# Kernel tuning notes

Hardware: AMD Instinct MI355X
Metric: run time of the kernel (lower is better)

## Reference

```python
import jax, jax.numpy as jnp
import numpy as np

DIM = 384
COMP = 64          # mmcv CARAFEPack compressed_channels default
KK = 9             # up_kernel^2 (up_kernel=3)
S = 2              # scale_factor


def conv2d(x, w, b, pad):
    y = jax.lax.conv_general_dilated(
        x, w, window_strides=(1, 1), padding=((pad, pad), (pad, pad)),
        dimension_numbers=('NCHW', 'OIHW', 'NCHW'))
    return y + b[None, :, None, None]


def pixel_shuffle(x, s):
    b, c, h, w = x.shape
    x = x.reshape(b, c // (s * s), s, s, h, w)
    x = x.transpose(0, 1, 4, 2, 5, 3)  # b, c', h, s, w, s
    return x.reshape(b, c // (s * s), h * s, w * s)


def carafe_pack(x, cw, cb, ew, eb):
    # x: [b, c, h, w] -> [b, c, 2h, 2w]
    b, c, h, w = x.shape
    comp = conv2d(x, cw, cb, 0)          # [b, 64, h, w]
    mask = conv2d(comp, ew, eb, 1)       # [b, 36, h, w]
    mask = pixel_shuffle(mask, S)        # [b, 9, 2h, 2w]
    mask = jax.nn.softmax(mask, axis=1)  # normalize the 9 reassembly weights
    # unfold 3x3 neighborhoods of x (zero pad 1)
    xp = jnp.pad(x, ((0, 0), (0, 0), (1, 1), (1, 1)))
    patches = jnp.stack(
        [xp[:, :, di:di + h, dj:dj + w] for di in range(3) for dj in range(3)],
        axis=2)                          # [b, c, 9, h, w]
    # each high-res pixel (i,j) reads the low-res window at (i//2, j//2)
    mr = mask.reshape(b, KK, h, S, w, S)
    out = jnp.einsum('bckhw,bkhpwq->bchpwq', patches, mr)
    return out.reshape(b, c, h * S, w * S)


def bilinear_resize(x, h, w):
    b, c = x.shape[:2]
    return jax.image.resize(x, (b, c, h, w), method='bilinear')


def stage(src, guidance, cw, cb, ew, eb):
    h, w = src.shape[2], src.shape[3]
    g = bilinear_resize(guidance, h, w)
    up = carafe_pack(jnp.concatenate([src, g], axis=1), cw, cb, ew, eb)
    return up[:, :DIM]


def setup_inputs() -> dict:
    key = jax.random.key(0)
    ks = jax.random.split(key, 20)
    cin = DIM + 3
    d = {}
    d['source'] = jax.random.normal(ks[0], (4, DIM, 14, 14), jnp.float32)
    d['guidance'] = jax.random.normal(ks[1], (4, 3, 224, 224), jnp.float32)
    i = 2
    for name in ('up1', 'up2', 'up3', 'up4'):
        d[name + '_cw'] = jax.random.normal(ks[i], (COMP, cin, 1, 1), jnp.float32) / np.sqrt(cin); i += 1
        d[name + '_cb'] = jnp.zeros((COMP,), jnp.float32)
        d[name + '_ew'] = jax.random.normal(ks[i], (KK * S * S, COMP, 3, 3), jnp.float32) / np.sqrt(COMP * 9); i += 1
        d[name + '_eb'] = jnp.zeros((KK * S * S,), jnp.float32)
    d['proj_w'] = jax.random.normal(ks[i], (DIM, cin, 1, 1), jnp.float32) / np.sqrt(cin)
    d['proj_b'] = jnp.zeros((DIM,), jnp.float32)
    return d


def reference(source, guidance,
              up1_cw, up1_cb, up1_ew, up1_eb,
              up2_cw, up2_cb, up2_ew, up2_eb,
              up3_cw, up3_cb, up3_ew, up3_eb,
              up4_cw, up4_cb, up4_ew, up4_eb,
              proj_w, proj_b):
    s2 = stage(source, guidance, up1_cw, up1_cb, up1_ew, up1_eb)
    s4 = stage(s2, guidance, up2_cw, up2_cb, up2_ew, up2_eb)
    s8 = stage(s4, guidance, up3_cw, up3_cb, up3_ew, up3_eb)
    s16 = stage(s8, guidance, up4_cw, up4_cb, up4_ew, up4_eb)
    return conv2d(jnp.concatenate([s16, guidance], axis=1), proj_w, proj_b, 0)
```

## Files before the change

kernel.cpp:

```cpp
#include <hip/hip_runtime.h>
#include <cstdint>

#define BATCH 4
#define DIMC 384
#define CINC 387
#define COMPC 64
#define GSZ 224

typedef __attribute__((ext_vector_type(8))) short bf16x8;
typedef __attribute__((ext_vector_type(4))) short s16x4;
typedef __attribute__((ext_vector_type(4))) float f32x4;

static __device__ __forceinline__ unsigned short f2bf(float x) {
  unsigned int u = __float_as_uint(x);
  unsigned int r = (u + 0x7fffu + ((u >> 16) & 1u)) >> 16;
  return (unsigned short)r;
}
static __device__ __forceinline__ float bf2f(unsigned short b) {
  return __uint_as_float(((unsigned int)b) << 16);
}
static __device__ __forceinline__ void cvt2(float x, unsigned short& h, unsigned short& l) {
  unsigned int u = __float_as_uint(x);
  unsigned int hb = (u + 0x7fffu + ((u >> 16) & 1u)) >> 16;
  h = (unsigned short)hb;
  float r = x - __uint_as_float(hb << 16);
  unsigned int u2 = __float_as_uint(r);
  l = (unsigned short)((u2 + 0x7fffu + ((u2 >> 16) & 1u)) >> 16);
}

__global__ void resize_all(const float* __restrict__ g, float* __restrict__ o0,
                           float* __restrict__ o1, float* __restrict__ o2,
                           float* __restrict__ o3) {
  int s = blockIdx.y;
  int h = 14 << s;
  float* out = (s == 0) ? o0 : (s == 1) ? o1 : (s == 2) ? o2 : o3;
  int inv_scale = GSZ / h;
  int w = h;
  int idx = blockIdx.x * blockDim.x + threadIdx.x;
  int total = BATCH * 3 * h * w;
  if (idx >= total) return;
  int j = idx % w; int t = idx / w;
  int i = t % h; t /= h;
  float ks = (float)inv_scale;
  float sy = (i + 0.5f) * ks - 0.5f;
  float sx = (j + 0.5f) * ks - 0.5f;
  int y0 = (int)ceilf(sy - ks); if (y0 < 0) y0 = 0;
  int y1 = (int)floorf(sy + ks); if (y1 > GSZ - 1) y1 = GSZ - 1;
  int x0 = (int)ceilf(sx - ks); if (x0 < 0) x0 = 0;
  int x1 = (int)floorf(sx + ks); if (x1 > GSZ - 1) x1 = GSZ - 1;
  const float* gp = g + (size_t)t * GSZ * GSZ;
  float wsx = 0.f;
  for (int x = x0; x <= x1; ++x) wsx += fmaxf(0.f, 1.f - fabsf(sx - (float)x) / ks);
  float acc = 0.f, wsy = 0.f;
  for (int y = y0; y <= y1; ++y) {
    float wy = fmaxf(0.f, 1.f - fabsf(sy - (float)y) / ks);
    wsy += wy;
    if (wy > 0.f) {
      const float* rp = gp + (size_t)y * GSZ;
      float row = 0.f;
      for (int x = x0; x <= x1; ++x) {
        float wx = fmaxf(0.f, 1.f - fabsf(sx - (float)x) / ks);
        row += wx * rp[x];
      }
      acc += wy * row;
    }
  }
  out[idx] = acc / (wsx * wsy);
}

__global__ void prep_cw(const float* __restrict__ c0, const float* __restrict__ c1,
                        const float* __restrict__ c2, const float* __restrict__ c3,
                        float* __restrict__ cwT) {
  int s = blockIdx.y;
  const float* cw = (s == 0) ? c0 : (s == 1) ? c1 : (s == 2) ? c2 : c3;
  int idx = blockIdx.x * 256 + threadIdx.x;
  if (idx >= CINC * COMPC) return;
  int ci = idx >> 6, co = idx & 63;
  cwT[s * (CINC * COMPC) + idx] = cw[co * CINC + ci];
}

#define EW2_PER_S (4 * COMPC * 9 * 12)
__global__ void prep_ew(const float* __restrict__ e0, const float* __restrict__ e1,
                        const float* __restrict__ e2, const float* __restrict__ e3,
                        float* __restrict__ ewT2) {
  int s = blockIdx.y;
  const float* ew = (s == 0) ? e0 : (s == 1) ? e1 : (s == 2) ? e2 : e3;
  int idx = blockIdx.x * 256 + threadIdx.x;
  if (idx >= EW2_PER_S) return;
  int k = idx % 12; int r = idx / 12;
  int tap = r % 9; r /= 9;
  int ci = r % COMPC; int pos = r / COMPC;
  float val = 0.f;
  if (k < 9) val = ew[(size_t)(k * 4 + pos) * (COMPC * 9) + ci * 9 + tap];
  ewT2[(size_t)s * EW2_PER_S + idx] = val;
}

#define KPAD 416
__global__ void prep_w(const float* __restrict__ pw, short* __restrict__ Whi,
                       short* __restrict__ Wlo) {
  int idx = blockIdx.x * 256 + threadIdx.x;
  if (idx >= DIMC * KPAD) return;
  int co = idx / KPAD, k = idx % KPAD;
  float v = (k < CINC) ? pw[co * CINC + k] : 0.f;
  unsigned short hb = f2bf(v);
  Whi[idx] = (short)hb;
  Wlo[idx] = (short)f2bf(v - bf2f(hb));
}

__global__ void comp_conv_kernel(const float* __restrict__ src, const float* __restrict__ g,
                                 const float* __restrict__ cwT, const float* __restrict__ cb,
                                 float* __restrict__ comp, int h, int w) {
  int hw = h * w;
  int p = blockIdx.x * 256 + threadIdx.x;
  if (p >= hw) return;
  int co0 = blockIdx.y * 32;
  int n = blockIdx.z;
  float acc[32];
  #pragma unroll
  for (int c = 0; c < 32; ++c) acc[c] = cb[co0 + c];
  const float* sp = src + (size_t)n * DIMC * hw + p;
  const float* wbase = cwT + co0;
  for (int ci = 0; ci < DIMC; ++ci) {
    float v = sp[(size_t)ci * hw];
    const float* wr = wbase + ci * COMPC;
    #pragma unroll
    for (int c = 0; c < 32; c += 4) {
      float4 wv = *(const float4*)(wr + c);
      acc[c] += wv.x * v; acc[c + 1] += wv.y * v;
      acc[c + 2] += wv.z * v; acc[c + 3] += wv.w * v;
    }
  }
  const float* gp = g + (size_t)n * 3 * hw + p;
  #pragma unroll
  for (int ci = 0; ci < 3; ++ci) {
    float v = gp[(size_t)ci * hw];
    const float* wr = wbase + (DIMC + ci) * COMPC;
    #pragma unroll
    for (int c = 0; c < 32; c += 4) {
      float4 wv = *(const float4*)(wr + c);
      acc[c] += wv.x * v; acc[c + 1] += wv.y * v;
      acc[c + 2] += wv.z * v; acc[c + 3] += wv.w * v;
    }
  }
  float* op = comp + (size_t)n * COMPC * hw + p;
  #pragma unroll
  for (int c = 0; c < 32; ++c) op[(size_t)(co0 + c) * hw] = acc[c];
}

__global__ void enc_mask_kernel(const float* __restrict__ comp, const float* __restrict__ ewT2,
                                const float* __restrict__ eb, float* __restrict__ mask,
                                int h, int w) {
  int hw = h * w;
  int sw2 = w >> 1;
  int nstrip = h * sw2;
  int strip = blockIdx.x * 256 + threadIdx.x;
  if (strip >= nstrip) return;
  int pos = blockIdx.y;
  int n = blockIdx.z;
  int i = strip / sw2;
  int j0 = (strip - i * sw2) * 2;
  float acc[2][9];
  #pragma unroll
  for (int k = 0; k < 9; ++k) {
    float bv = eb[k * 4 + pos];
    acc[0][k] = bv; acc[1][k] = bv;
  }
  const float* cpn = comp + (size_t)n * COMPC * hw;
  const float* wpos = ewT2 + (size_t)pos * COMPC * 9 * 12;
  for (int ci = 0; ci < COMPC; ++ci) {
    const float* cp = cpn + (size_t)ci * hw;
    float v[3][4];
    #pragma unroll
    for (int di = 0; di < 3; ++di) {
      int y = i + di - 1;
      bool yok = (y >= 0 && y < h);
      #pragma unroll
      for (int xx = 0; xx < 4; ++xx) {
        int x = j0 - 1 + xx;
        v[di][xx] = (yok && x >= 0 && x < w) ? cp[(size_t)y * w + x] : 0.f;
      }
    }
    const float* wb = wpos + (size_t)ci * 9 * 12;
    #pragma unroll
    for (int tap = 0; tap < 9; ++tap) {
      int di = tap / 3, dj = tap % 3;
      float4 wa = *(const float4*)(wb + tap * 12);
      float4 wc = *(const float4*)(wb + tap * 12 + 4);
      float w8 = wb[tap * 12 + 8];
      #pragma unroll
      for (int px = 0; px < 2; ++px) {
        float val = v[di][dj + px];
        acc[px][0] += wa.x * val; acc[px][1] += wa.y * val;
        acc[px][2] += wa.z * val; acc[px][3] += wa.w * val;
        acc[px][4] += wc.x * val; acc[px][5] += wc.y * val;
        acc[px][6] += wc.z * val; acc[px][7] += wc.w * val;
        acc[px][8] += w8 * val;
      }
    }
  }
  int pp = pos >> 1, q = pos & 1;
  int H = 2 * h, W = 2 * w;
  #pragma unroll
  for (int px = 0; px < 2; ++px) {
    int jj = j0 + px;
    float m = -1e30f;
    #pragma unroll
    for (int k = 0; k < 9; ++k) m = fmaxf(m, acc[px][k]);
    float e[9]; float s = 0.f;
    #pragma unroll
    for (int k = 0; k < 9; ++k) { e[k] = __expf(acc[px][k] - m); s += e[k]; }
    float inv = 1.f / s;
    float* mp = mask + (((size_t)n * H + (2 * i + pp)) * W + (2 * jj + q)) * 9;
    #pragma unroll
    for (int k = 0; k < 9; ++k) mp[k] = e[k] * inv;
  }
}

__global__ void carafe_kernel(const float* __restrict__ src, const float* __restrict__ mask,
                              float* __restrict__ out, int h, int w) {
  int p = blockIdx.x * blockDim.x + threadIdx.x;
  int hw = h * w;
  if (p >= hw) return;
  int c0 = blockIdx.y * 48, n = blockIdx.z;
  int i = p / w, j = p % w;
  int H = 2 * h, W = 2 * w;
  float m[4][9];
  #pragma unroll
  for (int pp = 0; pp < 2; ++pp)
    #pragma unroll
    for (int q = 0; q < 2; ++q) {
      const float* mp = mask + (((size_t)n * H + (2 * i + pp)) * W + (2 * j + q)) * 9;
      #pragma unroll
      for (int k = 0; k < 9; ++k) m[pp * 2 + q][k] = mp[k];
    }
  for (int cc = 0; cc < 48; ++cc) {
    int c = c0 + cc;
    const float* sp = src + ((size_t)(n * DIMC + c)) * hw;
    float v[9];
    #pragma unroll
    for (int k = 0; k < 9; ++k) {
      int y = i - 1 + k / 3, x = j - 1 + k % 3;
      v[k] = (y >= 0 && y < h && x >= 0 && x < w) ? sp[(size_t)y * w + x] : 0.f;
    }
    float* op = out + ((size_t)(n * DIMC + c)) * H * W;
    #pragma unroll
    for (int pp = 0; pp < 2; ++pp) {
      float a0 = 0.f, a1 = 0.f;
      #pragma unroll
      for (int k = 0; k < 9; ++k) {
        a0 += v[k] * m[pp * 2 + 0][k];
        a1 += v[k] * m[pp * 2 + 1][k];
      }
      float2 r; r.x = a0; r.y = a1;
      *(float2*)(op + (size_t)(2 * i + pp) * W + 2 * j) = r;
    }
  }
}

__global__ __launch_bounds__(512, 4) void final_conv_mfma4(
    const float* __restrict__ guid, const short* __restrict__ Whi,
    const short* __restrict__ Wlo, const float* __restrict__ pb,
    float* __restrict__ out) {
  __shared__ short XH[2][2048];
  __shared__ short XL[2][2048];
  const int HW = GSZ * GSZ;
  const int n = blockIdx.y;
  const int px0 = blockIdx.x * 64;
  const int tid = threadIdx.x;
  const int wv = tid >> 6;
  const int lane = tid & 63;
  const int lm = lane & 15, qq = lane >> 4;

  const int s_nt = lane >> 4, s_lm = lane & 15;
  const int s_qq = wv >> 1;
  const int s_jh = (wv & 1) * 4;
  const int waddr = ((s_nt * 4 + s_qq) * 16 + s_lm) * 8 + s_jh;

  const float* Xb = out + (size_t)n * DIMC * HW + px0 + lane;
  const float* Gb = guid + (size_t)n * 3 * HW + px0 + lane;

  f32x4 acc[3][4];
  #pragma unroll
  for (int mt = 0; mt < 3; ++mt)
    #pragma unroll
    for (int nt = 0; nt < 4; ++nt) acc[mt][nt] = (f32x4){0.f, 0.f, 0.f, 0.f};

  float nvA[4];
  bf16x8 ahC[3], alC[3];
  {
    unsigned short hs[4], ls[4];
    #pragma unroll
    for (int i = 0; i < 4; ++i) {
      float v = Xb[(size_t)(wv * 4 + i) * HW];
      cvt2(v, hs[i], ls[i]);
    }
    *(s16x4*)&XH[0][waddr] = (s16x4){(short)hs[0], (short)hs[1], (short)hs[2], (short)hs[3]};
    *(s16x4*)&XL[0][waddr] = (s16x4){(short)ls[0], (short)ls[1], (short)ls[2], (short)ls[3]};
    #pragma unroll
    for (int i = 0; i < 4; ++i) nvA[i] = Xb[(size_t)(32 + wv * 4 + i) * HW];
    #pragma unroll
    for (int mt = 0; mt < 3; ++mt) {
      int co = wv * 48 + mt * 16 + lm;
      size_t woff = (size_t)co * KPAD + qq * 8;
      ahC[mt] = *(const bf16x8*)(Whi + woff);
      alC[mt] = *(const bf16x8*)(Wlo + woff);
    }
  }
  __syncthreads();

  #pragma unroll
  for (int kt = 0; kt < 13; ++kt) {
    const int cur = kt & 1;
    bf16x8 ahN[3], alN[3];
    if (kt < 12) {
      #pragma unroll
      for (int mt = 0; mt < 3; ++mt) {
        int co = wv * 48 + mt * 16 + lm;
        size_t woff = (size_t)co * KPAD + (kt + 1) * 32 + qq * 8;
        ahN[mt] = *(const bf16x8*)(Whi + woff);
        alN[mt] = *(const bf16x8*)(Wlo + woff);
      }
    }
    float nvB[4] = {0.f, 0.f, 0.f, 0.f};
    if (kt <= 10) {
      int kb = (kt + 2) * 32 + wv * 4;
      if (kt < 10) {
        #pragma unroll
        for (int i = 0; i < 4; ++i) nvB[i] = Xb[(size_t)(kb + i) * HW];
      } else {
        #pragma unroll
        for (int i = 0; i < 4; ++i) {
          int k = kb + i;
          nvB[i] = (k < CINC) ? Gb[(size_t)(k - DIMC) * HW] : 0.f;
        }
      }
    }
    #pragma unroll
    for (int nt = 0; nt < 4; ++nt) {
      int a = ((nt * 4 + qq) * 16 + lm) * 8;
      bf16x8 bh = *(const bf16x8*)&XH[cur][a];
      bf16x8 bl = *(const bf16x8*)&XL[cur][a];
      #pragma unroll
      for (int mt = 0; mt < 3; ++mt) {
        acc[mt][nt] = __builtin_amdgcn_mfma_f32_16x16x32_bf16(ahC[mt], bh, acc[mt][nt], 0, 0, 0);
        acc[mt][nt] = __builtin_amdgcn_mfma_f32_16x16x32_bf16(ahC[mt], bl, acc[mt][nt], 0, 0, 0);
        acc[mt][nt] = __builtin_amdgcn_mfma_f32_16x16x32_bf16(alC[mt], bh, acc[mt][nt], 0, 0, 0);
      }
    }
    if (kt <= 11) {
      unsigned short hs[4], ls[4];
      #pragma unroll
      for (int i = 0; i < 4; ++i) cvt2(nvA[i], hs[i], ls[i]);
      *(s16x4*)&XH[cur ^ 1][waddr] = (s16x4){(short)hs[0], (short)hs[1], (short)hs[2], (short)hs[3]};
      *(s16x4*)&XL[cur ^ 1][waddr] = (s16x4){(short)ls[0], (short)ls[1], (short)ls[2], (short)ls[3]};
    }
    asm volatile("s_waitcnt lgkmcnt(0)" ::: "memory");
    __builtin_amdgcn_s_barrier();
    __builtin_amdgcn_sched_barrier(0);
    #pragma unroll
    for (int i = 0; i < 4; ++i) nvA[i] = nvB[i];
    if (kt < 12) {
      #pragma unroll
      for (int mt = 0; mt < 3; ++mt) { ahC[mt] = ahN[mt]; alC[mt] = alN[mt]; }
    }
  }

  #pragma unroll
  for (int mt = 0; mt < 3; ++mt) {
    #pragma unroll
    for (int nt = 0; nt < 4; ++nt) {
      #pragma unroll
      for (int r = 0; r < 4; ++r) {
        int co = wv * 48 + mt * 16 + qq * 4 + r;
        int px = px0 + nt * 16 + lm;
        out[((size_t)(n * DIMC + co)) * HW + px] = acc[mt][nt][r] + pb[co];
      }
    }
  }
}

extern "C" void kernel_launch(void* const* d_in, const int* in_sizes, int n_in,
                              void* d_out, int out_size, void* d_ws, size_t ws_size,
                              hipStream_t stream) {
  const float* source   = (const float*)d_in[0];
  const float* guidance = (const float*)d_in[1];
  const float* cw[4] = {(const float*)d_in[2],  (const float*)d_in[6],
                        (const float*)d_in[10], (const float*)d_in[14]};
  const float* cb[4] = {(const float*)d_in[3],  (const float*)d_in[7],
                        (const float*)d_in[11], (const float*)d_in[15]};
  const float* ew[4] = {(const float*)d_in[4],  (const float*)d_in[8],
                        (const float*)d_in[12], (const float*)d_in[16]};
  const float* eb[4] = {(const float*)d_in[5],  (const float*)d_in[9],
                        (const float*)d_in[13], (const float*)d_in[17]};
  const float* pw = (const float*)d_in[18];
  const float* pb = (const float*)d_in[19];
  float* out = (float*)d_out;

  float* ws = (float*)d_ws;
  float* g14  = ws;
  float* g28  = g14 + 2352;
  float* g56  = g28 + 9408;
  float* g112 = g56 + 37632;
  float* comp_buf = g112 + 150528;
  float* mask_buf = comp_buf + 3211264;
  float* s2  = mask_buf + 1806336;
  float* s4  = s2 + 1204224;
  float* s8  = s4 + 4816896;
  float* cwT = s8 + 19267584;
  float* ewT2 = cwT + 99072;
  short* Whi = (short*)(ewT2 + 110592);
  short* Wlo = Whi + DIMC * KPAD;

  prep_cw<<<dim3((CINC * COMPC + 255) / 256, 4), 256, 0, stream>>>(cw[0], cw[1], cw[2], cw[3], cwT);
  prep_ew<<<dim3((EW2_PER_S + 255) / 256, 4), 256, 0, stream>>>(ew[0], ew[1], ew[2], ew[3], ewT2);
  prep_w<<<(DIMC * KPAD + 255) / 256, 256, 0, stream>>>(pw, Whi, Wlo);
  resize_all<<<dim3((BATCH * 3 * 112 * 112 + 255) / 256, 4), 256, 0, stream>>>(
      guidance, g14, g28, g56, g112);

  const float* srcs[4] = {source, s2, s4, s8};
  float* outs[4] = {s2, s4, s8, out};
  float* gbufs[4] = {g14, g28, g56, g112};
  const int hs[4] = {14, 28, 56, 112};
  for (int s = 0; s < 4; ++s) {
    int h = hs[s], w = h, hw = h * w;
    int sw2 = w / 2;
    comp_conv_kernel<<<dim3((hw + 255) / 256, 2, BATCH), 256, 0, stream>>>(
        srcs[s], gbufs[s], cwT + s * (CINC * COMPC), cb[s], comp_buf, h, w);
    enc_mask_kernel<<<dim3((h * sw2 + 255) / 256, 4, BATCH), 256, 0, stream>>>(
        comp_buf, ewT2 + (size_t)s * EW2_PER_S, eb[s], mask_buf, h, w);
    carafe_kernel<<<dim3((hw + 255) / 256, DIMC / 48, BATCH), 256, 0, stream>>>(
        srcs[s], mask_buf, outs[s], h, w);
  }
  final_conv_mfma4<<<dim3((GSZ * GSZ) / 64, BATCH), 512, 0, stream>>>(guidance, Whi, Wlo, pb, out);
}
```

Measured before the change: 1.644 ms.

## Merge prep kernels, stage weights in LDS, template sizes, restructure final conv loop

Folds the four preprocessing kernels into one launch. It stages the compression and encoder weights in shared memory per block and templates the stage kernels on spatial size so indexing is compile-time. The final MFMA conv now loads A fragments per k-tile instead of prefetching them one step ahead, and uses a plain __syncthreads. This cuts launch count and repeated global weight reads, but the final conv loses its A-operand prefetch, which may expose load latency.

```diff
diff --git a/kernel.cpp b/kernel.cpp
--- a/kernel.cpp
+++ b/kernel.cpp
@@ -28,101 +28,107 @@
   l = (unsigned short)((u2 + 0x7fffu + ((u2 >> 16) & 1u)) >> 16);
 }
 
-__global__ void resize_all(const float* __restrict__ g, float* __restrict__ o0,
-                           float* __restrict__ o1, float* __restrict__ o2,
-                           float* __restrict__ o3) {
-  int s = blockIdx.y;
-  int h = 14 << s;
-  float* out = (s == 0) ? o0 : (s == 1) ? o1 : (s == 2) ? o2 : o3;
-  int inv_scale = GSZ / h;
-  int w = h;
-  int idx = blockIdx.x * blockDim.x + threadIdx.x;
-  int total = BATCH * 3 * h * w;
-  if (idx >= total) return;
-  int j = idx % w; int t = idx / w;
-  int i = t % h; t /= h;
-  float ks = (float)inv_scale;
-  float sy = (i + 0.5f) * ks - 0.5f;
-  float sx = (j + 0.5f) * ks - 0.5f;
-  int y0 = (int)ceilf(sy - ks); if (y0 < 0) y0 = 0;
-  int y1 = (int)floorf(sy + ks); if (y1 > GSZ - 1) y1 = GSZ - 1;
-  int x0 = (int)ceilf(sx - ks); if (x0 < 0) x0 = 0;
-  int x1 = (int)floorf(sx + ks); if (x1 > GSZ - 1) x1 = GSZ - 1;
-  const float* gp = g + (size_t)t * GSZ * GSZ;
-  float wsx = 0.f;
-  for (int x = x0; x <= x1; ++x) wsx += fmaxf(0.f, 1.f - fabsf(sx - (float)x) / ks);
-  float acc = 0.f, wsy = 0.f;
-  for (int y = y0; y <= y1; ++y) {
-    float wy = fmaxf(0.f, 1.f - fabsf(sy - (float)y) / ks);
-    wsy += wy;
-    if (wy > 0.f) {
-      const float* rp = gp + (size_t)y * GSZ;
-      float row = 0.f;
-      for (int x = x0; x <= x1; ++x) {
-        float wx = fmaxf(0.f, 1.f - fabsf(sx - (float)x) / ks);
-        row += wx * rp[x];
-      }
-      acc += wy * row;
-    }
-  }
-  out[idx] = acc / (wsx * wsy);
-}
-
-__global__ void prep_cw(const float* __restrict__ c0, const float* __restrict__ c1,
-                        const float* __restrict__ c2, const float* __restrict__ c3,
-                        float* __restrict__ cwT) {
-  int s = blockIdx.y;
-  const float* cw = (s == 0) ? c0 : (s == 1) ? c1 : (s == 2) ? c2 : c3;
+#define KPAD 416
+#define EW2_PER_S (4 * COMPC * 9 * 12)
+
+__global__ void prep_all(const float* __restrict__ c0, const float* __restrict__ c1,
+                         const float* __restrict__ c2, const float* __restrict__ c3,
+                         const float* __restrict__ e0, const float* __restrict__ e1,
+                         const float* __restrict__ e2, const float* __restrict__ e3,
+                         const float* __restrict__ pw,
+                         float* __restrict__ cwT, float* __restrict__ ewT2,
+                         short* __restrict__ Whi, short* __restrict__ Wlo,
+                         const float* __restrict__ g,
+                         float* __restrict__ r0, float* __restrict__ r1,
+                         float* __restrict__ r2, float* __restrict__ r3) {
+  int type = blockIdx.y;
   int idx = blockIdx.x * 256 + threadIdx.x;
-  if (idx >= CINC * COMPC) return;
-  int ci = idx >> 6, co = idx & 63;
-  cwT[s * (CINC * COMPC) + idx] = cw[co * CINC + ci];
-}
-
-#define EW2_PER_S (4 * COMPC * 9 * 12)
-__global__ void prep_ew(const float* __restrict__ e0, const float* __restrict__ e1,
-                        const float* __restrict__ e2, const float* __restrict__ e3,
-                        float* __restrict__ ewT2) {
-  int s = blockIdx.y;
-  const float* ew = (s == 0) ? e0 : (s == 1) ? e1 : (s == 2) ? e2 : e3;
-  int idx = blockIdx.x * 256 + threadIdx.x;
-  if (idx >= EW2_PER_S) return;
-  int k = idx % 12; int r = idx / 12;
-  int tap = r % 9; r /= 9;
-  int ci = r % COMPC; int pos = r / COMPC;
-  float val = 0.f;
-  if (k < 9) val = ew[(size_t)(k * 4 + pos) * (COMPC * 9) + ci * 9 + tap];
-  ewT2[(size_t)s * EW2_PER_S + idx] = val;
-}
-
-#define KPAD 416
-__global__ void prep_w(const float* __restrict__ pw, short* __restrict__ Whi,
-                       short* __restrict__ Wlo) {
-  int idx = blockIdx.x * 256 + threadIdx.x;
-  if (idx >= DIMC * KPAD) return;
-  int co = idx / KPAD, k = idx % KPAD;
-  float v = (k < CINC) ? pw[co * CINC + k] : 0.f;
-  unsigned short hb = f2bf(v);
-  Whi[idx] = (short)hb;
-  Wlo[idx] = (short)f2bf(v - bf2f(hb));
-}
-
+  if (type == 0) {
+    if (idx >= 4 * CINC * COMPC) return;
+    int s = idx / (CINC * COMPC), r = idx % (CINC * COMPC);
+    const float* cw = (s == 0) ? c0 : (s == 1) ? c1 : (s == 2) ? c2 : c3;
+    int ci = r >> 6, co = r & 63;
+    cwT[idx] = cw[co * CINC + ci];
+  } else if (type == 1) {
+    if (idx >= 4 * EW2_PER_S) return;
+    int s = idx / EW2_PER_S, r = idx % EW2_PER_S;
+    const float* ew = (s == 0) ? e0 : (s == 1) ? e1 : (s == 2) ? e2 : e3;
+    int k = r % 12; int rr = r / 12;
+    int tap = rr % 9; rr /= 9;
+    int ci = rr % COMPC; int pos = rr / COMPC;
+    float val = 0.f;
+    if (k < 9) val = ew[(size_t)(k * 4 + pos) * (COMPC * 9) + ci * 9 + tap];
+    ewT2[idx] = val;
+  } else if (type == 2) {
+    if (idx >= DIMC * KPAD) return;
+    int co = idx / KPAD, k = idx % KPAD;
+    float v = (k < CINC) ? pw[co * CINC + k] : 0.f;
+    unsigned short hb = f2bf(v);
+    Whi[idx] = (short)hb;
+    Wlo[idx] = (short)f2bf(v - bf2f(hb));
+  } else {
+    int s, base;
+    if (idx < 2352)        { s = 0; base = 0; }
+    else if (idx < 11760)  { s = 1; base = 2352; }
+    else if (idx < 49392)  { s = 2; base = 11760; }
+    else if (idx < 199920) { s = 3; base = 49392; }
+    else return;
+    int h = 14 << s, w = h;
+    float* out = (s == 0) ? r0 : (s == 1) ? r1 : (s == 2) ? r2 : r3;
+    int inv_scale = GSZ / h;
+    int local = idx - base;
+    int j = local % w; int t = local / w;
+    int i = t % h; t /= h;
+    float ks = (float)inv_scale;
+    float sy = (i + 0.5f) * ks - 0.5f;
+    float sx = (j + 0.5f) * ks - 0.5f;
+    int y0 = (int)ceilf(sy - ks); if (y0 < 0) y0 = 0;
+    int y1 = (int)floorf(sy + ks); if (y1 > GSZ - 1) y1 = GSZ - 1;
+    int x0 = (int)ceilf(sx - ks); if (x0 < 0) x0 = 0;
+    int x1 = (int)floorf(sx + ks); if (x1 > GSZ - 1) x1 = GSZ - 1;
+    const float* gp = g + (size_t)t * GSZ * GSZ;
+    float wsx = 0.f;
+    for (int x = x0; x <= x1; ++x) wsx += fmaxf(0.f, 1.f - fabsf(sx - (float)x) / ks);
+    float acc = 0.f, wsy = 0.f;
+    for (int y = y0; y <= y1; ++y) {
+      float wy = fmaxf(0.f, 1.f - fabsf(sy - (float)y) / ks);
+      wsy += wy;
+      if (wy > 0.f) {
+        const float* rp = gp + (size_t)y * GSZ;
+        float row = 0.f;
+        for (int x = x0; x <= x1; ++x) {
+          float wx = fmaxf(0.f, 1.f - fabsf(sx - (float)x) / ks);
+          row += wx * rp[x];
+        }
+        acc += wy * row;
+      }
+    }
+    out[local] = acc / (wsx * wsy);
+  }
+}
+
+template <int H>
 __global__ void comp_conv_kernel(const float* __restrict__ src, const float* __restrict__ g,
                                  const float* __restrict__ cwT, const float* __restrict__ cb,
-                                 float* __restrict__ comp, int h, int w) {
-  int hw = h * w;
+                                 float* __restrict__ comp) {
+  constexpr int hw = H * H;
+  __shared__ __align__(16) float WL[CINC * 32];
+  int co0 = blockIdx.y * 32;
+  for (int idx = threadIdx.x; idx < CINC * 32; idx += 256) {
+    int ci = idx >> 5, c = idx & 31;
+    WL[idx] = cwT[ci * COMPC + co0 + c];
+  }
+  __syncthreads();
   int p = blockIdx.x * 256 + threadIdx.x;
   if (p >= hw) return;
-  int co0 = blockIdx.y * 32;
   int n = blockIdx.z;
   float acc[32];
   #pragma unroll
   for (int c = 0; c < 32; ++c) acc[c] = cb[co0 + c];
   const float* sp = src + (size_t)n * DIMC * hw + p;
-  const float* wbase = cwT + co0;
   for (int ci = 0; ci < DIMC; ++ci) {
     float v = sp[(size_t)ci * hw];
-    const float* wr = wbase + ci * COMPC;
+    const float* wr = &WL[ci * 32];
     #pragma unroll
     for (int c = 0; c < 32; c += 4) {
       float4 wv = *(const float4*)(wr + c);
@@ -134,7 +140,7 @@
   #pragma unroll
   for (int ci = 0; ci < 3; ++ci) {
     float v = gp[(size_t)ci * hw];
-    const float* wr = wbase + (DIMC + ci) * COMPC;
+    const float* wr = &WL[(DIMC + ci) * 32];
     #pragma unroll
     for (int c = 0; c < 32; c += 4) {
       float4 wv = *(const float4*)(wr + c);
@@ -147,12 +153,18 @@
   for (int c = 0; c < 32; ++c) op[(size_t)(co0 + c) * hw] = acc[c];
 }
 
+template <int H>
 __global__ void enc_mask_kernel(const float* __restrict__ comp, const float* __restrict__ ewT2,
-                                const float* __restrict__ eb, float* __restrict__ mask,
-                                int h, int w) {
-  int hw = h * w;
-  int sw2 = w >> 1;
-  int nstrip = h * sw2;
+                                const float* __restrict__ eb, float* __restrict__ mask) {
+  constexpr int hw = H * H;
+  constexpr int sw2 = H / 2;
+  constexpr int nstrip = H * sw2;
+  __shared__ __align__(16) float WL[COMPC * 9 * 12];
+  {
+    const float* wpos = ewT2 + (size_t)blockIdx.y * (COMPC * 9 * 12);
+    for (int idx = threadIdx.x; idx < COMPC * 9 * 12; idx += 256) WL[idx] = wpos[idx];
+  }
+  __syncthreads();
   int strip = blockIdx.x * 256 + threadIdx.x;
   if (strip >= nstrip) return;
   int pos = blockIdx.y;
@@ -166,21 +178,20 @@
     acc[0][k] = bv; acc[1][k] = bv;
   }
   const float* cpn = comp + (size_t)n * COMPC * hw;
-  const float* wpos = ewT2 + (size_t)pos * COMPC * 9 * 12;
   for (int ci = 0; ci < COMPC; ++ci) {
     const float* cp = cpn + (size_t)ci * hw;
     float v[3][4];
     #pragma unroll
     for (int di = 0; di < 3; ++di) {
       int y = i + di - 1;
-      bool yok = (y >= 0 && y < h);
+      bool yok = (y >= 0 && y < H);
       #pragma unroll
       for (int xx = 0; xx < 4; ++xx) {
         int x = j0 - 1 + xx;
-        v[di][xx] = (yok && x >= 0 && x < w) ? cp[(size_t)y * w + x] : 0.f;
-      }
-    }
-    const float* wb = wpos + (size_t)ci * 9 * 12;
+        v[di][xx] = (yok && x >= 0 && x < H) ? cp[(size_t)y * H + x] : 0.f;
+      }
+    }
+    const float* wb = &WL[ci * 108];
     #pragma unroll
     for (int tap = 0; tap < 9; ++tap) {
       int di = tap / 3, dj = tap % 3;
@@ -199,7 +210,7 @@
     }
   }
   int pp = pos >> 1, q = pos & 1;
-  int H = 2 * h, W = 2 * w;
+  constexpr int W = 2 * H;
   #pragma unroll
   for (int px = 0; px < 2; ++px) {
     int jj = j0 + px;
@@ -210,26 +221,27 @@
     #pragma unroll
     for (int k = 0; k < 9; ++k) { e[k] = __expf(acc[px][k] - m); s += e[k]; }
     float inv = 1.f / s;
-    float* mp = mask + (((size_t)n * H + (2 * i + pp)) * W + (2 * jj + q)) * 9;
+    float* mp = mask + (((size_t)n * W + (2 * i + pp)) * W + (2 * jj + q)) * 9;
     #pragma unroll
     for (int k = 0; k < 9; ++k) mp[k] = e[k] * inv;
   }
 }
 
+template <int H>
 __global__ void carafe_kernel(const float* __restrict__ src, const float* __restrict__ mask,
-                              float* __restrict__ out, int h, int w) {
+                              float* __restrict__ out) {
+  constexpr int hw = H * H;
+  constexpr int W = 2 * H;
   int p = blockIdx.x * blockDim.x + threadIdx.x;
-  int hw = h * w;
   if (p >= hw) return;
   int c0 = blockIdx.y * 48, n = blockIdx.z;
-  int i = p / w, j = p % w;
-  int H = 2 * h, W = 2 * w;
+  int i = p / H, j = p % H;
   float m[4][9];
   #pragma unroll
   for (int pp = 0; pp < 2; ++pp)
     #pragma unroll
     for (int q = 0; q < 2; ++q) {
-      const float* mp = mask + (((size_t)n * H + (2 * i + pp)) * W + (2 * j + q)) * 9;
+      const float* mp = mask + (((size_t)n * W + (2 * i + pp)) * W + (2 * j + q)) * 9;
       #pragma unroll
       for (int k = 0; k < 9; ++k) m[pp * 2 + q][k] = mp[k];
     }
@@ -240,9 +252,9 @@
     #pragma unroll
     for (int k = 0; k < 9; ++k) {
       int y = i - 1 + k / 3, x = j - 1 + k % 3;
-      v[k] = (y >= 0 && y < h && x >= 0 && x < w) ? sp[(size_t)y * w + x] : 0.f;
-    }
-    float* op = out + ((size_t)(n * DIMC + c)) * H * W;
+      v[k] = (y >= 0 && y < H && x >= 0 && x < H) ? sp[(size_t)y * H + x] : 0.f;
+    }
+    float* op = out + ((size_t)(n * DIMC + c)) * W * W;
     #pragma unroll
     for (int pp = 0; pp < 2; ++pp) {
       float a0 = 0.f, a1 = 0.f;
@@ -257,7 +269,7 @@
   }
 }
 
-__global__ __launch_bounds__(512, 4) void final_conv_mfma4(
+__global__ __launch_bounds__(512, 4) void final_conv_mfma3(
     const float* __restrict__ guid, const short* __restrict__ Whi,
     const short* __restrict__ Wlo, const float* __restrict__ pb,
     float* __restrict__ out) {
@@ -286,7 +298,6 @@
     for (int nt = 0; nt < 4; ++nt) acc[mt][nt] = (f32x4){0.f, 0.f, 0.f, 0.f};
 
   float nvA[4];
-  bf16x8 ahC[3], alC[3];
   {
     unsigned short hs[4], ls[4];
     #pragma unroll
@@ -298,29 +309,32 @@
     *(s16x4*)&XL[0][waddr] = (s16x4){(short)ls[0], (short)ls[1], (short)ls[2], (short)ls[3]};
     #pragma unroll
     for (int i = 0; i < 4; ++i) nvA[i] = Xb[(size_t)(32 + wv * 4 + i) * HW];
+  }
+  __syncthreads();
+
+  for (int kt = 0; kt < 13; ++kt) {
+    const int cur = kt & 1;
+    bf16x8 bh[4], bl[4];
+    #pragma unroll
+    for (int nt = 0; nt < 4; ++nt) {
+      int a = ((nt * 4 + qq) * 16 + lm) * 8;
+      bh[nt] = *(const bf16x8*)&XH[cur][a];
+      bl[nt] = *(const bf16x8*)&XL[cur][a];
+    }
     #pragma unroll
     for (int mt = 0; mt < 3; ++mt) {
       int co = wv * 48 + mt * 16 + lm;
-      size_t woff = (size_t)co * KPAD + qq * 8;
-      ahC[mt] = *(const bf16x8*)(Whi + woff);
-      alC[mt] = *(const bf16x8*)(Wlo + woff);
-    }
-  }
-  __syncthreads();
-
-  #pragma unroll
-  for (int kt = 0; kt < 13; ++kt) {
-    const int cur = kt & 1;
-    bf16x8 ahN[3], alN[3];
-    if (kt < 12) {
-      #pragma unroll
-      for (int mt = 0; mt < 3; ++mt) {
-        int co = wv * 48 + mt * 16 + lm;
-        size_t woff = (size_t)co * KPAD + (kt + 1) * 32 + qq * 8;
-        ahN[mt] = *(const bf16x8*)(Whi + woff);
-        alN[mt] = *(const bf16x8*)(Wlo + woff);
-      }
-    }
+      size_t woff = (size_t)co * KPAD + kt * 32 + qq * 8;
+      bf16x8 ah = *(const bf16x8*)(Whi + woff);
+      bf16x8 al = *(const bf16x8*)(Wlo + woff);
+      #pragma unroll
+      for (int nt = 0; nt < 4; ++nt) {
+        acc[mt][nt] = __builtin_amdgcn_mfma_f32_16x16x32_bf16(ah, bh[nt], acc[mt][nt], 0, 0, 0);
+        acc[mt][nt] = __builtin_amdgcn_mfma_f32_16x16x32_bf16(ah, bl[nt], acc[mt][nt], 0, 0, 0);
+        acc[mt][nt] = __builtin_amdgcn_mfma_f32_16x16x32_bf16(al, bh[nt], acc[mt][nt], 0, 0, 0);
+      }
+    }
+    __builtin_amdgcn_sched_barrier(0);
     float nvB[4] = {0.f, 0.f, 0.f, 0.f};
     if (kt <= 10) {
       int kb = (kt + 2) * 32 + wv * 4;
@@ -335,18 +349,6 @@
         }
       }
     }
-    #pragma unroll
-    for (int nt = 0; nt < 4; ++nt) {
-      int a = ((nt * 4 + qq) * 16 + lm) * 8;
-      bf16x8 bh = *(const bf16x8*)&XH[cur][a];
-      bf16x8 bl = *(const bf16x8*)&XL[cur][a];
-      #pragma unroll
-      for (int mt = 0; mt < 3; ++mt) {
-        acc[mt][nt] = __builtin_amdgcn_mfma_f32_16x16x32_bf16(ahC[mt], bh, acc[mt][nt], 0, 0, 0);
-        acc[mt][nt] = __builtin_amdgcn_mfma_f32_16x16x32_bf16(ahC[mt], bl, acc[mt][nt], 0, 0, 0);
-        acc[mt][nt] = __builtin_amdgcn_mfma_f32_16x16x32_bf16(alC[mt], bh, acc[mt][nt], 0, 0, 0);
-      }
-    }
     if (kt <= 11) {
       unsigned short hs[4], ls[4];
       #pragma unroll
@@ -354,15 +356,9 @@
       *(s16x4*)&XH[cur ^ 1][waddr] = (s16x4){(short)hs[0], (short)hs[1], (short)hs[2], (short)hs[3]};
       *(s16x4*)&XL[cur ^ 1][waddr] = (s16x4){(short)ls[0], (short)ls[1], (short)ls[2], (short)ls[3]};
     }
-    asm volatile("s_waitcnt lgkmcnt(0)" ::: "memory");
-    __builtin_amdgcn_s_barrier();
-    __builtin_amdgcn_sched_barrier(0);
+    __syncthreads();
     #pragma unroll
     for (int i = 0; i < 4; ++i) nvA[i] = nvB[i];
-    if (kt < 12) {
-      #pragma unroll
-      for (int mt = 0; mt < 3; ++mt) { ahC[mt] = ahN[mt]; alC[mt] = alN[mt]; }
-    }
   }
 
   #pragma unroll
@@ -411,25 +407,35 @@
   short* Whi = (short*)(ewT2 + 110592);
   short* Wlo = Whi + DIMC * KPAD;
 
-  prep_cw<<<dim3((CINC * COMPC + 255) / 256, 4), 256, 0, stream>>>(cw[0], cw[1], cw[2], cw[3], cwT);
-  prep_ew<<<dim3((EW2_PER_S + 255) / 256, 4), 256, 0, stream>>>(ew[0], ew[1], ew[2], ew[3], ewT2);
-  prep_w<<<(DIMC * KPAD + 255) / 256, 256, 0, stream>>>(pw, Whi, Wlo);
-  resize_all<<<dim3((BATCH * 3 * 112 * 112 + 255) / 256, 4), 256, 0, stream>>>(
-      guidance, g14, g28, g56, g112);
-
-  const float* srcs[4] = {source, s2, s4, s8};
-  float* outs[4] = {s2, s4, s8, out};
-  float* gbufs[4] = {g14, g28, g56, g112};
-  const int hs[4] = {14, 28, 56, 112};
-  for (int s = 0; s < 4; ++s) {
-    int h = hs[s], w = h, hw = h * w;
-    int sw2 = w / 2;
-    comp_conv_kernel<<<dim3((hw + 255) / 256, 2, BATCH), 256, 0, stream>>>(
-        srcs[s], gbufs[s], cwT + s * (CINC * COMPC), cb[s], comp_buf, h, w);
-    enc_mask_kernel<<<dim3((h * sw2 + 255) / 256, 4, BATCH), 256, 0, stream>>>(
-        comp_buf, ewT2 + (size_t)s * EW2_PER_S, eb[s], mask_buf, h, w);
-    carafe_kernel<<<dim3((hw + 255) / 256, DIMC / 48, BATCH), 256, 0, stream>>>(
-        srcs[s], mask_buf, outs[s], h, w);
-  }
-  final_conv_mfma4<<<dim3((GSZ * GSZ) / 64, BATCH), 512, 0, stream>>>(guidance, Whi, Wlo, pb, out);
-}
+  prep_all<<<dim3(782, 4), 256, 0, stream>>>(
+      cw[0], cw[1], cw[2], cw[3], ew[0], ew[1], ew[2], ew[3], pw,
+      cwT, ewT2, Whi, Wlo, guidance, g14, g28, g56, g112);
+
+  comp_conv_kernel<14><<<dim3(1, 2, BATCH), 256, 0, stream>>>(
+      source, g14, cwT + 0 * (CINC * COMPC), cb[0], comp_buf);
+  enc_mask_kernel<14><<<dim3(1, 4, BATCH), 256, 0, stream>>>(
+      comp_buf, ewT2 + 0 * (size_t)EW2_PER_S, eb[0], mask_buf);
+  carafe_kernel<14><<<dim3(1, DIMC / 48, BATCH), 256, 0, stream>>>(
+      source, mask_buf, s2);
+  comp_conv_kernel<28><<<dim3(4, 2, BATCH), 256, 0, stream>>>(
+      s2, g28, cwT + 1 * (CINC * COMPC), cb[1], comp_buf);
+  enc_mask_kernel<28><<<dim3(2, 4, BATCH), 256, 0, stream>>>(
+      comp_buf, ewT2 + 1 * (size_t)EW2_PER_S, eb[1], mask_buf);
+  carafe_kernel<28><<<dim3(4, DIMC / 48, BATCH), 256, 0, stream>>>(
+      s2, mask_buf, s4);
+  comp_conv_kernel<56><<<dim3(13, 2, BATCH), 256, 0, stream>>>(
+      s4, g56, cwT + 2 * (CINC * COMPC), cb[2], comp_buf);
+  enc_mask_kernel<56><<<dim3(7, 4, BATCH), 256, 0, stream>>>(
+      comp_buf, ewT2 + 2 * (size_t)EW2_PER_S, eb[2], mask_buf);
+  carafe_kernel<56><<<dim3(13, DIMC / 48, BATCH), 256, 0, stream>>>(
+      s4, mask_buf, s8);
+  comp_conv_kernel<112><<<dim3(49, 2, BATCH), 256, 0, stream>>>(
+      s8, g112, cwT + 3 * (CINC * COMPC), cb[3], comp_buf);
+  enc_mask_kernel<112><<<dim3(25, 4, BATCH), 256, 0, stream>>>(
+      comp_buf, ewT2 + 3 * (size_t)EW2_PER_S, eb[3], mask_buf);
+  carafe_kernel<112><<<dim3(49, DIMC / 48, BATCH), 256, 0, stream>>>(
+      s8, mask_buf, out);
+
+  final_conv_mfma3<<<dim3((GSZ * GSZ) / 64, BATCH), 512, 0, stream>>>(
+      guidance, Whi, Wlo, pb, out);
+}
```

Result: faster. 1.425 ms (-13.3%).
